# Performance work log

Hardware: AMD Instinct MI355X
Metric: run time of the kernel (lower is better)

The kernel has to match this reference:

```python
import jax, jax.numpy as jnp
import numpy as np


def setup_inputs() -> dict:
    key = jax.random.key(0)
    k1, k2 = jax.random.split(key)
    D = 512
    B, N = 32, 512
    panel_embeddings = jax.random.normal(k1, (B, N, D), dtype=jnp.float32)
    # nn.Bilinear(D, D, 1) weight: (1, D, D) -> squeeze to (D, D); bias: scalar
    bound = 1.0 / np.sqrt(D)
    W = jax.random.uniform(k2, (D, D), dtype=jnp.float32, minval=-bound, maxval=bound)
    b = jnp.float32(0.0)
    return {"panel_embeddings": panel_embeddings, "W": W, "b": b}


def reference(panel_embeddings, W, b):
    # score[b,i,j] = x_i^T W x_j + b, with diagonal forced to 0 (loop skips i==j)
    xw = jnp.einsum('bid,de->bie', panel_embeddings, W)          # (B, N, D)
    scores = jnp.einsum('bie,bje->bij', xw, panel_embeddings) + b  # (B, N, N)
    N = panel_embeddings.shape[1]
    mask = ~jnp.eye(N, dtype=bool)
    return jnp.where(mask, scores, jnp.zeros_like(scores))
```

## Files before the change

### kernel.cpp

```cpp
#include <hip/hip_runtime.h>
#include <stdint.h>

#define BATCH 32
#define NDIM 512
#define DDIM 512
#define XELEMS (BATCH * NDIM * DDIM)
#define WELEMS (DDIM * DDIM)

typedef _Float16 f16x8 __attribute__((ext_vector_type(8)));
typedef _Float16 f16x4v __attribute__((ext_vector_type(4)));
typedef float f32x4 __attribute__((ext_vector_type(4)));

__device__ __forceinline__ void gl_lds16(const _Float16* g, _Float16* l) {
    __builtin_amdgcn_global_load_lds(
        (const __attribute__((address_space(1))) unsigned int*)(g),
        (__attribute__((address_space(3))) unsigned int*)(l),
        16, 0, 0);
}

__global__ __launch_bounds__(256) void prep(const float4* __restrict__ X4,
                                            f16x4v* __restrict__ Xh4,
                                            const float* __restrict__ W,
                                            _Float16* __restrict__ Wt) {
    __shared__ float tile[32][33];
    int bid = blockIdx.x;
    if (bid < XELEMS / 4 / 256) {
        int i = bid * 256 + threadIdx.x;
        float4 v = X4[i];
        f16x4v o;
        o.x = (_Float16)v.x;
        o.y = (_Float16)v.y;
        o.z = (_Float16)v.z;
        o.w = (_Float16)v.w;
        Xh4[i] = o;
    } else {
        int t = bid - XELEMS / 4 / 256;
        int bx = t & 15;
        int by = t >> 4;
        int tx = threadIdx.x & 31;
        int ty = threadIdx.x >> 5;
        for (int r = ty; r < 32; r += 8)
            tile[r][tx] = W[(by * 32 + r) * DDIM + bx * 32 + tx];
        __syncthreads();
        for (int r = ty; r < 32; r += 8)
            Wt[(size_t)(bx * 32 + r) * DDIM + by * 32 + tx] = (_Float16)tile[tx][r];
    }
}

__global__ __launch_bounds__(512) void fused(const _Float16* __restrict__ Xh,
                                             const _Float16* __restrict__ Wt,
                                             float* __restrict__ Sout,
                                             const float* __restrict__ bias_ptr) {
    __shared__ __align__(16) _Float16 Ylds[64 * 512];
    __shared__ __align__(16) _Float16 As2[2][64 * 32];
    __shared__ __align__(16) _Float16 Bs2[2][512 * 32];

    const int tid  = threadIdx.x;
    const int lane = tid & 63;
    const int wv   = tid >> 6;
    const int quad = lane >> 4;
    const int l16  = lane & 15;

    const int lr2 = lane >> 2;
    const int lc2 = lane & 3;
    const int lk2 = (lc2 ^ ((lr2 >> 1) & 3)) * 8;

    const int paK = (quad ^ ((l16 >> 1) & 3)) * 8;

    const int blk   = blockIdx.x;
    const int batch = blk & 31;
    const int r0    = (blk >> 5) * 64;

    const _Float16* Xb = Xh + (size_t)batch * (NDIM * DDIM);

    f32x4 acc[4][4];
#pragma unroll
    for (int i = 0; i < 4; ++i)
#pragma unroll
        for (int j = 0; j < 4; ++j)
            acc[i][j] = (f32x4){0.f, 0.f, 0.f, 0.f};

    if (wv < 4)
        gl_lds16(Xb + (size_t)(r0 + wv * 16 + lr2) * DDIM + lk2, &As2[0][wv * 512]);
#pragma unroll
    for (int t = 0; t < 4; ++t) {
        const int chunk = wv * 4 + t;
        gl_lds16(Wt + (size_t)(chunk * 16 + lr2) * DDIM + lk2, &Bs2[0][chunk * 512]);
    }
    __syncthreads();

    int buf = 0;
    for (int it = 0; it < 16; ++it) {
        if (it < 15) {
            const int k0 = (it + 1) * 32;
            if (wv < 4)
                gl_lds16(Xb + (size_t)(r0 + wv * 16 + lr2) * DDIM + k0 + lk2,
                         &As2[buf ^ 1][wv * 512]);
#pragma unroll
            for (int t = 0; t < 4; ++t) {
                const int chunk = wv * 4 + t;
                gl_lds16(Wt + (size_t)(chunk * 16 + lr2) * DDIM + k0 + lk2,
                         &Bs2[buf ^ 1][chunk * 512]);
            }
        } else {
#pragma unroll
            for (int t = 0; t < 4; ++t) {
                const int chunk = wv * 4 + t;
                gl_lds16(Xb + (size_t)(chunk * 16 + lr2) * DDIM + lk2,
                         &Bs2[buf ^ 1][chunk * 512]);
            }
        }

        {
            f16x8 a[4], b[4];
#pragma unroll
            for (int mt = 0; mt < 4; ++mt)
                a[mt] = *(const f16x8*)&As2[buf][(mt * 16 + l16) * 32 + paK];
#pragma unroll
            for (int nt = 0; nt < 4; ++nt)
                b[nt] = *(const f16x8*)&Bs2[buf][(wv * 64 + nt * 16 + l16) * 32 + paK];
#pragma unroll
            for (int mt = 0; mt < 4; ++mt)
#pragma unroll
                for (int nt = 0; nt < 4; ++nt)
                    acc[mt][nt] = __builtin_amdgcn_mfma_f32_16x16x32_f16(
                        a[mt], b[nt], acc[mt][nt], 0, 0, 0);
        }
        __syncthreads();
        buf ^= 1;
    }

#pragma unroll
    for (int mt = 0; mt < 4; ++mt)
#pragma unroll
        for (int nt = 0; nt < 4; ++nt)
#pragma unroll
            for (int r = 0; r < 4; ++r) {
                int i = mt * 16 + quad * 4 + r;
                int e = wv * 64 + nt * 16 + l16;
                int c = e >> 3, j = e & 7;
                Ylds[i * 512 + (((c ^ (i & 7)) << 3) | j)] = (_Float16)acc[mt][nt][r];
            }
    __syncthreads();

#pragma unroll
    for (int i = 0; i < 4; ++i)
#pragma unroll
        for (int j = 0; j < 4; ++j)
            acc[i][j] = (f32x4){0.f, 0.f, 0.f, 0.f};

    for (int it = 0; it < 16; ++it) {
        if (it < 15) {
            const int e0 = (it + 1) * 32;
#pragma unroll
            for (int t = 0; t < 4; ++t) {
                const int chunk = wv * 4 + t;
                gl_lds16(Xb + (size_t)(chunk * 16 + lr2) * DDIM + e0 + lk2,
                         &Bs2[buf ^ 1][chunk * 512]);
            }
        }

        {
            const int pay = (((it * 4 + quad) ^ (l16 & 7)) * 8);
            f16x8 a[4], b[4];
#pragma unroll
            for (int mt = 0; mt < 4; ++mt)
                a[mt] = *(const f16x8*)&Ylds[(mt * 16 + l16) * 512 + pay];
#pragma unroll
            for (int nt = 0; nt < 4; ++nt)
                b[nt] = *(const f16x8*)&Bs2[buf][(wv * 64 + nt * 16 + l16) * 32 + paK];
#pragma unroll
            for (int mt = 0; mt < 4; ++mt)
#pragma unroll
                for (int nt = 0; nt < 4; ++nt)
                    acc[mt][nt] = __builtin_amdgcn_mfma_f32_16x16x32_f16(
                        a[mt], b[nt], acc[mt][nt], 0, 0, 0);
        }
        __syncthreads();
        buf ^= 1;
    }

    const float bias = bias_ptr[0];
#pragma unroll
    for (int mt = 0; mt < 4; ++mt)
#pragma unroll
        for (int nt = 0; nt < 4; ++nt)
#pragma unroll
            for (int r = 0; r < 4; ++r) {
                int gi = r0 + mt * 16 + quad * 4 + r;
                int gj = wv * 64 + nt * 16 + l16;
                float v = acc[mt][nt][r] + bias;
                if (gi == gj) v = 0.f;
                Sout[((size_t)batch * NDIM + gi) * NDIM + gj] = v;
            }
}

extern "C" void kernel_launch(void* const* d_in, const int* in_sizes, int n_in,
                              void* d_out, int out_size, void* d_ws, size_t ws_size,
                              hipStream_t stream) {
    const float* X  = (const float*)d_in[0];
    const float* W  = (const float*)d_in[1];
    const float* bp = (const float*)d_in[2];
    float* out = (float*)d_out;

    _Float16* Xh = (_Float16*)d_ws;
    _Float16* Wt = Xh + XELEMS;

    prep<<<XELEMS / 4 / 256 + 256, 256, 0, stream>>>((const float4*)X, (f16x4v*)Xh, W, Wt);

    fused<<<256, 512, 0, stream>>>(Xh, Wt, out, bp);

    (void)in_sizes; (void)n_in; (void)out_size; (void)ws_size;
}
```

Before: 120.7 us.

## Fuse fp32-to-fp16 conversion of X into GEMM kernel and load operands directly to registers

Removes the separate pass that converts all of X to fp16 in workspace. The fused kernel now reads fp32 X directly, converting the A tile into LDS once and converting B fragments in registers. W and X operand fragments are loaded straight from global memory into registers with one-step prefetch instead of double-buffered LDS staging, which drops per-iteration barriers and shrinks LDS to a single 64KB buffer, with launch bounds requesting 2 blocks per CU. In exchange, each wave issues uncoalesced-ish per-lane global loads and reads twice the bytes for X in fp32, and register pressure rises.

```diff
diff --git a/kernel.cpp b/kernel.cpp
--- a/kernel.cpp
+++ b/kernel.cpp
@@ -4,56 +4,40 @@
 #define BATCH 32
 #define NDIM 512
 #define DDIM 512
-#define XELEMS (BATCH * NDIM * DDIM)
 #define WELEMS (DDIM * DDIM)
 
 typedef _Float16 f16x8 __attribute__((ext_vector_type(8)));
-typedef _Float16 f16x4v __attribute__((ext_vector_type(4)));
 typedef float f32x4 __attribute__((ext_vector_type(4)));
 
-__device__ __forceinline__ void gl_lds16(const _Float16* g, _Float16* l) {
-    __builtin_amdgcn_global_load_lds(
-        (const __attribute__((address_space(1))) unsigned int*)(g),
-        (__attribute__((address_space(3))) unsigned int*)(l),
-        16, 0, 0);
-}
-
-__global__ __launch_bounds__(256) void prep(const float4* __restrict__ X4,
-                                            f16x4v* __restrict__ Xh4,
-                                            const float* __restrict__ W,
-                                            _Float16* __restrict__ Wt) {
+__device__ __forceinline__ f16x8 cvt8(float4 u0, float4 u1) {
+    f16x8 r;
+    r[0] = (_Float16)u0.x; r[1] = (_Float16)u0.y;
+    r[2] = (_Float16)u0.z; r[3] = (_Float16)u0.w;
+    r[4] = (_Float16)u1.x; r[5] = (_Float16)u1.y;
+    r[6] = (_Float16)u1.z; r[7] = (_Float16)u1.w;
+    return r;
+}
+
+__global__ __launch_bounds__(256) void prep_wt(const float* __restrict__ W,
+                                               _Float16* __restrict__ Wt) {
     __shared__ float tile[32][33];
-    int bid = blockIdx.x;
-    if (bid < XELEMS / 4 / 256) {
-        int i = bid * 256 + threadIdx.x;
-        float4 v = X4[i];
-        f16x4v o;
-        o.x = (_Float16)v.x;
-        o.y = (_Float16)v.y;
-        o.z = (_Float16)v.z;
-        o.w = (_Float16)v.w;
-        Xh4[i] = o;
-    } else {
-        int t = bid - XELEMS / 4 / 256;
-        int bx = t & 15;
-        int by = t >> 4;
-        int tx = threadIdx.x & 31;
-        int ty = threadIdx.x >> 5;
-        for (int r = ty; r < 32; r += 8)
-            tile[r][tx] = W[(by * 32 + r) * DDIM + bx * 32 + tx];
-        __syncthreads();
-        for (int r = ty; r < 32; r += 8)
-            Wt[(size_t)(bx * 32 + r) * DDIM + by * 32 + tx] = (_Float16)tile[tx][r];
-    }
-}
-
-__global__ __launch_bounds__(512) void fused(const _Float16* __restrict__ Xh,
-                                             const _Float16* __restrict__ Wt,
-                                             float* __restrict__ Sout,
-                                             const float* __restrict__ bias_ptr) {
-    __shared__ __align__(16) _Float16 Ylds[64 * 512];
-    __shared__ __align__(16) _Float16 As2[2][64 * 32];
-    __shared__ __align__(16) _Float16 Bs2[2][512 * 32];
+    int t = blockIdx.x;
+    int bx = t & 15;
+    int by = t >> 4;
+    int tx = threadIdx.x & 31;
+    int ty = threadIdx.x >> 5;
+    for (int r = ty; r < 32; r += 8)
+        tile[r][tx] = W[(by * 32 + r) * DDIM + bx * 32 + tx];
+    __syncthreads();
+    for (int r = ty; r < 32; r += 8)
+        Wt[(size_t)(bx * 32 + r) * DDIM + by * 32 + tx] = (_Float16)tile[tx][r];
+}
+
+__global__ __launch_bounds__(512, 2) void fused(const float* __restrict__ X,
+                                                const _Float16* __restrict__ Wt,
+                                                float* __restrict__ Sout,
+                                                const float* __restrict__ bias_ptr) {
+    __shared__ __align__(16) _Float16 AY[64 * 512];
 
     const int tid  = threadIdx.x;
     const int lane = tid & 63;
@@ -64,14 +48,22 @@
     const int lr2 = lane >> 2;
     const int lc2 = lane & 3;
     const int lk2 = (lc2 ^ ((lr2 >> 1) & 3)) * 8;
-
     const int paK = (quad ^ ((l16 >> 1) & 3)) * 8;
 
     const int blk   = blockIdx.x;
     const int batch = blk & 31;
     const int r0    = (blk >> 5) * 64;
 
-    const _Float16* Xb = Xh + (size_t)batch * (NDIM * DDIM);
+    const float* Xb = X + (size_t)batch * (NDIM * DDIM);
+
+    const _Float16* gb1[4];
+    const float*    gb2[4];
+#pragma unroll
+    for (int nt = 0; nt < 4; ++nt) {
+        const int row = wv * 64 + nt * 16 + l16;
+        gb1[nt] = Wt + (size_t)row * DDIM + quad * 8;
+        gb2[nt] = Xb + (size_t)row * DDIM + quad * 8;
+    }
 
     f32x4 acc[4][4];
 #pragma unroll
@@ -80,56 +72,47 @@
         for (int j = 0; j < 4; ++j)
             acc[i][j] = (f32x4){0.f, 0.f, 0.f, 0.f};
 
-    if (wv < 4)
-        gl_lds16(Xb + (size_t)(r0 + wv * 16 + lr2) * DDIM + lk2, &As2[0][wv * 512]);
-#pragma unroll
-    for (int t = 0; t < 4; ++t) {
-        const int chunk = wv * 4 + t;
-        gl_lds16(Wt + (size_t)(chunk * 16 + lr2) * DDIM + lk2, &Bs2[0][chunk * 512]);
-    }
-    __syncthreads();
-
-    int buf = 0;
+    f16x8 bb[4];
+#pragma unroll
+    for (int nt = 0; nt < 4; ++nt)
+        bb[nt] = *(const f16x8*)(gb1[nt]);
+#pragma unroll
+    for (int c = 0; c < 8; ++c) {
+        const int kt = wv * 2 + (c >> 2);
+        const int rc = c & 3;
+        const float* g = Xb + (size_t)(r0 + rc * 16 + lr2) * DDIM + kt * 32 + lk2;
+        float4 u0 = *(const float4*)g;
+        float4 u1 = *(const float4*)(g + 4);
+        *(f16x8*)&AY[(kt * 4 + rc) * 512 + lr2 * 32 + lc2 * 8] = cvt8(u0, u1);
+    }
+    __syncthreads();
+
+#pragma unroll
     for (int it = 0; it < 16; ++it) {
-        if (it < 15) {
-            const int k0 = (it + 1) * 32;
-            if (wv < 4)
-                gl_lds16(Xb + (size_t)(r0 + wv * 16 + lr2) * DDIM + k0 + lk2,
-                         &As2[buf ^ 1][wv * 512]);
-#pragma unroll
-            for (int t = 0; t < 4; ++t) {
-                const int chunk = wv * 4 + t;
-                gl_lds16(Wt + (size_t)(chunk * 16 + lr2) * DDIM + k0 + lk2,
-                         &Bs2[buf ^ 1][chunk * 512]);
-            }
-        } else {
-#pragma unroll
-            for (int t = 0; t < 4; ++t) {
-                const int chunk = wv * 4 + t;
-                gl_lds16(Xb + (size_t)(chunk * 16 + lr2) * DDIM + lk2,
-                         &Bs2[buf ^ 1][chunk * 512]);
-            }
-        }
-
-        {
-            f16x8 a[4], b[4];
-#pragma unroll
-            for (int mt = 0; mt < 4; ++mt)
-                a[mt] = *(const f16x8*)&As2[buf][(mt * 16 + l16) * 32 + paK];
-#pragma unroll
-            for (int nt = 0; nt < 4; ++nt)
-                b[nt] = *(const f16x8*)&Bs2[buf][(wv * 64 + nt * 16 + l16) * 32 + paK];
-#pragma unroll
-            for (int mt = 0; mt < 4; ++mt)
-#pragma unroll
-                for (int nt = 0; nt < 4; ++nt)
-                    acc[mt][nt] = __builtin_amdgcn_mfma_f32_16x16x32_f16(
-                        a[mt], b[nt], acc[mt][nt], 0, 0, 0);
-        }
-        __syncthreads();
-        buf ^= 1;
-    }
-
+        f16x8 bn[4];
+        if (it < 15) {
+#pragma unroll
+            for (int nt = 0; nt < 4; ++nt)
+                bn[nt] = *(const f16x8*)(gb1[nt] + (it + 1) * 32);
+        }
+        f16x8 a[4];
+#pragma unroll
+        for (int mt = 0; mt < 4; ++mt)
+            a[mt] = *(const f16x8*)&AY[(it * 4 + mt) * 512 + l16 * 32 + paK];
+#pragma unroll
+        for (int mt = 0; mt < 4; ++mt)
+#pragma unroll
+            for (int nt = 0; nt < 4; ++nt)
+                acc[mt][nt] = __builtin_amdgcn_mfma_f32_16x16x32_f16(
+                    a[mt], bb[nt], acc[mt][nt], 0, 0, 0);
+        if (it < 15) {
+#pragma unroll
+            for (int nt = 0; nt < 4; ++nt)
+                bb[nt] = bn[nt];
+        }
+    }
+
+    __syncthreads();
 #pragma unroll
     for (int mt = 0; mt < 4; ++mt)
 #pragma unroll
@@ -139,7 +122,7 @@
                 int i = mt * 16 + quad * 4 + r;
                 int e = wv * 64 + nt * 16 + l16;
                 int c = e >> 3, j = e & 7;
-                Ylds[i * 512 + (((c ^ (i & 7)) << 3) | j)] = (_Float16)acc[mt][nt][r];
+                AY[i * 512 + (((c ^ (i & 7)) << 3) | j)] = (_Float16)acc[mt][nt][r];
             }
     __syncthreads();
 
@@ -149,35 +132,44 @@
         for (int j = 0; j < 4; ++j)
             acc[i][j] = (f32x4){0.f, 0.f, 0.f, 0.f};
 
+    float4 c0[4], c1[4];
+#pragma unroll
+    for (int nt = 0; nt < 4; ++nt) {
+        c0[nt] = *(const float4*)(gb2[nt]);
+        c1[nt] = *(const float4*)(gb2[nt] + 4);
+    }
+#pragma unroll
     for (int it = 0; it < 16; ++it) {
-        if (it < 15) {
-            const int e0 = (it + 1) * 32;
-#pragma unroll
-            for (int t = 0; t < 4; ++t) {
-                const int chunk = wv * 4 + t;
-                gl_lds16(Xb + (size_t)(chunk * 16 + lr2) * DDIM + e0 + lk2,
-                         &Bs2[buf ^ 1][chunk * 512]);
-            }
-        }
-
-        {
-            const int pay = (((it * 4 + quad) ^ (l16 & 7)) * 8);
-            f16x8 a[4], b[4];
-#pragma unroll
-            for (int mt = 0; mt < 4; ++mt)
-                a[mt] = *(const f16x8*)&Ylds[(mt * 16 + l16) * 512 + pay];
-#pragma unroll
-            for (int nt = 0; nt < 4; ++nt)
-                b[nt] = *(const f16x8*)&Bs2[buf][(wv * 64 + nt * 16 + l16) * 32 + paK];
-#pragma unroll
-            for (int mt = 0; mt < 4; ++mt)
-#pragma unroll
-                for (int nt = 0; nt < 4; ++nt)
-                    acc[mt][nt] = __builtin_amdgcn_mfma_f32_16x16x32_f16(
-                        a[mt], b[nt], acc[mt][nt], 0, 0, 0);
-        }
-        __syncthreads();
-        buf ^= 1;
+        float4 n0[4], n1[4];
+        if (it < 15) {
+#pragma unroll
+            for (int nt = 0; nt < 4; ++nt) {
+                n0[nt] = *(const float4*)(gb2[nt] + (it + 1) * 32);
+                n1[nt] = *(const float4*)(gb2[nt] + (it + 1) * 32 + 4);
+            }
+        }
+        f16x8 b[4];
+#pragma unroll
+        for (int nt = 0; nt < 4; ++nt)
+            b[nt] = cvt8(c0[nt], c1[nt]);
+        const int pay = (((it * 4 + quad) ^ (l16 & 7)) * 8);
+        f16x8 a[4];
+#pragma unroll
+        for (int mt = 0; mt < 4; ++mt)
+            a[mt] = *(const f16x8*)&AY[(mt * 16 + l16) * 512 + pay];
+#pragma unroll
+        for (int mt = 0; mt < 4; ++mt)
+#pragma unroll
+            for (int nt = 0; nt < 4; ++nt)
+                acc[mt][nt] = __builtin_amdgcn_mfma_f32_16x16x32_f16(
+                    a[mt], b[nt], acc[mt][nt], 0, 0, 0);
+        if (it < 15) {
+#pragma unroll
+            for (int nt = 0; nt < 4; ++nt) {
+                c0[nt] = n0[nt];
+                c1[nt] = n1[nt];
+            }
+        }
     }
 
     const float bias = bias_ptr[0];
@@ -203,12 +195,11 @@
     const float* bp = (const float*)d_in[2];
     float* out = (float*)d_out;
 
-    _Float16* Xh = (_Float16*)d_ws;
-    _Float16* Wt = Xh + XELEMS;
-
-    prep<<<XELEMS / 4 / 256 + 256, 256, 0, stream>>>((const float4*)X, (f16x4v*)Xh, W, Wt);
-
-    fused<<<256, 512, 0, stream>>>(Xh, Wt, out, bp);
+    _Float16* Wt = (_Float16*)d_ws;
+
+    prep_wt<<<256, 256, 0, stream>>>(W, Wt);
+
+    fused<<<256, 512, 0, stream>>>(X, Wt, out, bp);
 
     (void)in_sizes; (void)n_in; (void)out_size; (void)ws_size;
 }
```

Result: slower. 132.7 us (+10.0%).
